# Kernel tuning notes

Hardware: AMD Instinct MI355X
Metric: run time of the kernel (lower is better)

Reference implementation:

```python
import jax, jax.numpy as jnp
import numpy as np

B, N = 256, 512          # trees, nodes per tree (topological order, root last)
IN, HID, OUT = 57, 512, 57  # len(ascii_letters + " .,;'") = 57


def setup_inputs() -> dict:
    rng = np.random.default_rng(0)
    # children indices strictly less than node index; -1 means absent child
    u = rng.random((B, N, 2))
    idx = np.arange(N)[None, :, None]
    ch = np.floor(u * (idx + 1)).astype(np.int32) - 1  # in [-1, i-1]
    left_idx = jnp.asarray(ch[..., 0])
    right_idx = jnp.asarray(ch[..., 1])
    values = jnp.asarray(rng.integers(0, IN, (B, N)), dtype=jnp.int32)
    key = jax.random.key(0)
    k1, k2, k3, k4 = jax.random.split(key, 4)
    s1 = 1.0 / np.sqrt(IN + HID)
    s2 = 1.0 / np.sqrt(HID)
    W_ih = jax.random.uniform(k1, (IN + HID, HID), minval=-s1, maxval=s1, dtype=jnp.float32)
    b_ih = jax.random.uniform(k2, (HID,), minval=-s1, maxval=s1, dtype=jnp.float32)
    W_o = jax.random.uniform(k3, (HID, OUT), minval=-s2, maxval=s2, dtype=jnp.float32)
    b_o = jax.random.uniform(k4, (OUT,), minval=-s2, maxval=s2, dtype=jnp.float32)
    return dict(left_idx=left_idx, right_idx=right_idx, values=values,
                W_ih=W_ih, b_ih=b_ih, W_o=W_o, b_o=b_o)


def _encode(left_idx, right_idx, values, W_ih, b_ih):
    # one-hot chars, precompute the input half of the concat+linear for all nodes
    X = jax.nn.one_hot(values, IN, dtype=W_ih.dtype)        # [B,N,IN]
    Wx, Wh = W_ih[:IN], W_ih[IN:]                            # split concat linear
    Xp = jnp.einsum('bni,ih->bnh', X, Wx) + b_ih             # [B,N,HID]
    SENT = N  # sentinel row holding zeros (hidden for None child)
    li = jnp.where(left_idx < 0, SENT, left_idx)             # [B,N]
    ri = jnp.where(right_idx < 0, SENT, right_idx)
    H0 = jnp.zeros((B, N + 1, HID), Xp.dtype)
    brange = jnp.arange(B)

    def step(H, inp):
        i, xp, l, r = inp                                    # xp:[B,HID], l/r:[B]
        hl = H[brange, l]                                    # gather child hiddens
        hr = H[brange, r]
        h = jnp.tanh(xp + (hl + hr) @ Wh)                    # recurrence
        H = H.at[:, i].set(h)
        return H, None

    xs = (jnp.arange(N), jnp.swapaxes(Xp, 0, 1), li.T, ri.T)
    H, _ = jax.lax.scan(step, H0, xs)
    return H[:, N - 1]                                       # root hidden [B,HID]


def reference(left_idx, right_idx, values, W_ih, b_ih, W_o, b_o):
    h_root = _encode(left_idx, right_idx, values, W_ih, b_ih)
    logits = h_root @ W_o + b_o                              # i2o
    return jax.nn.log_softmax(logits, axis=1)                # [B,OUT]
```

## Files before the change

kernel.cpp:

```cpp
#include <hip/hip_runtime.h>
#include <stdint.h>

#define BATCH 256
#define NNODE 512
#define INP   57
#define HIDD  512
#define OUTD  57

typedef int i32x4 __attribute__((ext_vector_type(4)));

__global__ void pack_wq(const float* __restrict__ W_ih, const float* __restrict__ b_ih,
                        signed char* __restrict__ Wq){
  int idx = blockIdx.x * 256 + threadIdx.x;
  int j    =  idx        & 15;
  int lane = (idx >> 4)  & 63;
  int nt   = (idx >> 10) & 31;
  int kt   =  idx >> 15;
  int n    = nt * 16 + (lane & 15);
  int ksub = (lane >> 4) * 16 + j;
  const float scale = 127.0f * sqrtf((float)(INP + HIDD));
  float wv; float sc = scale;
  if (kt < 8)            wv = W_ih[(size_t)(INP + kt * 64 + ksub) * HIDD + n];
  else {
    sc = scale * 0.5f;
    if (ksub < INP)      wv = W_ih[(size_t)ksub * HIDD + n];
    else if (ksub == INP) wv = b_ih[n];
    else                 wv = 0.0f;
  }
  float q = rintf(wv * sc);
  q = fminf(127.0f, fmaxf(-127.0f, q));
  Wq[idx] = (signed char)q;
}

__device__ __forceinline__ unsigned int avg_s8x4(unsigned int a, unsigned int b){
#if __has_builtin(__builtin_amdgcn_lerp)
  return __builtin_amdgcn_lerp(a ^ 0x80808080u, b ^ 0x80808080u, 0x01010101u) ^ 0x80808080u;
#else
  unsigned int au = a ^ 0x80808080u, bu = b ^ 0x80808080u;
  unsigned int o = au | bu, x = au ^ bu;
  return ((o - ((x >> 1) & 0x7F7F7F7Fu)) ^ 0x80808080u);
#endif
}

struct Pref { uint4 l[2]; uint4 r[2]; };

__device__ __forceinline__ Pref load_pref(
    int m0, int Mcur, int w, int m16, int quad,
    const int* ord_s, const int* li_s, const int* ri_s,
    const signed char* Hb)
{
  Pref p;
  const int koff = w * 64 + quad * 16;
  #pragma unroll
  for (int mt = 0; mt < 2; ++mt) {
    const int row  = mt * 16 + m16;
    const int node = (row < Mcur) ? ord_s[m0 + row] : -1;
    const int loff = (node >= 0) ? li_s[node] : NNODE * HIDD;
    p.l[mt] = *(const uint4*)(Hb + (size_t)(loff + koff));
    const int roff = (node >= 0) ? ri_s[node] : NNODE * HIDD;
    p.r[mt] = *(const uint4*)(Hb + (size_t)(roff + koff));
  }
  return p;
}

__device__ __forceinline__ void write_pref(
    const Pref& p, int m0, int Mcur, int w, int lane, int m16, int quad,
    signed char* __restrict__ Ab, const int* ord_s, const int* val_s)
{
  #pragma unroll
  for (int mt = 0; mt < 2; ++mt) {
    uint4 o;
    o.x = avg_s8x4(p.l[mt].x, p.r[mt].x);
    o.y = avg_s8x4(p.l[mt].y, p.r[mt].y);
    o.z = avg_s8x4(p.l[mt].z, p.r[mt].z);
    o.w = avg_s8x4(p.l[mt].w, p.r[mt].w);
    *(uint4*)(Ab + (w * 2 + mt) * 1024 + lane * 16) = o;
  }
  if (w < 2) {
    const int erow  = w * 16 + m16;
    const int enode = (erow < Mcur) ? ord_s[m0 + erow] : -1;
    const int v     = (enode >= 0) ? val_s[enode] : -1;
    signed char bytes[16];
    #pragma unroll
    for (int j = 0; j < 16; ++j) {
      const int ks = quad * 16 + j;
      bytes[j] = (enode >= 0 && (ks == v || ks == INP)) ? (signed char)127 : (signed char)0;
    }
    *(i32x4*)(Ab + (16 + w) * 1024 + lane * 16) = *(const i32x4*)bytes;
  }
}

template<int NMT>
__device__ __forceinline__ void compute_chunk(
    int m0, int Mcur, int w, int lane, int m16, int quad,
    const signed char* __restrict__ Ab,
    const int* ordoff_s, const i32x4 (&Bv)[9][4], signed char* Hb)
{
  i32x4 acc[NMT][4];
  #pragma unroll
  for (int mt = 0; mt < NMT; ++mt)
    #pragma unroll
    for (int nt = 0; nt < 4; ++nt)
      acc[mt][nt] = (i32x4){0, 0, 0, 0};

  #pragma unroll
  for (int kt = 0; kt < 8; ++kt) {
    #pragma unroll
    for (int mt = 0; mt < NMT; ++mt) {
      i32x4 a = *(const i32x4*)(Ab + (kt * 2 + mt) * 1024 + lane * 16);
      #pragma unroll
      for (int nt = 0; nt < 4; ++nt)
        acc[mt][nt] = __builtin_amdgcn_mfma_i32_16x16x64_i8(a, Bv[kt][nt], acc[mt][nt], 0, 0, 0);
    }
  }
  #pragma unroll
  for (int mt = 0; mt < NMT; ++mt) {
    i32x4 ax = *(const i32x4*)(Ab + (16 + mt) * 1024 + lane * 16);
    #pragma unroll
    for (int nt = 0; nt < 4; ++nt)
      acc[mt][nt] = __builtin_amdgcn_mfma_i32_16x16x64_i8(ax, Bv[8][nt], acc[mt][nt], 0, 0, 0);
  }

  const float SCLE = 5.7707801635558536f / (16129.0f * sqrtf((float)(INP + HIDD)));
  #pragma unroll
  for (int mt = 0; mt < NMT; ++mt) {
    #pragma unroll
    for (int rg = 0; rg < 4; ++rg) {
      const int rowc = mt * 16 + quad * 4 + rg;
      if (rowc < Mcur) {
        signed char* hp = Hb + (size_t)ordoff_s[m0 + rowc] + (w * 64 + m16);
        #pragma unroll
        for (int nt = 0; nt < 4; ++nt) {
          const float x  = (float)acc[mt][nt][rg] * SCLE;
          const float e  = __builtin_amdgcn_exp2f(x);
          const float r  = __builtin_amdgcn_rcpf(e + 1.0f);
          const float tq = fmaf(-254.0f, r, 127.0f);
          hp[nt * 16] = (signed char)__float2int_rn(tq);
        }
      }
    }
  }
}

__global__ __launch_bounds__(512, 2) void tree_rnn(
    const int* __restrict__ left, const int* __restrict__ right,
    const int* __restrict__ values,
    const float* __restrict__ W_ih, const float* __restrict__ b_ih,
    const float* __restrict__ W_o,  const float* __restrict__ b_o,
    const signed char* __restrict__ Wq,
    signed char* __restrict__ Hbuf, float* __restrict__ out)
{
  __shared__ __align__(16) signed char Abuf[2][18 * 1024];
  __shared__ int li_s[NNODE], ri_s[NNODE], val_s[NNODE];
  __shared__ int lvl_s[NNODE], ord_s[NNODE], ordoff_s[NNODE];
  __shared__ int cnt_s[NNODE], cnt2_s[NNODE];
  __shared__ int offs_s[NNODE + 1];
  __shared__ int chg_s, lmax_s;
  __shared__ float hroot_s[HIDD];
  __shared__ float red_s[OUTD][8];
  __shared__ float logit_s[64];

  const int b    = blockIdx.x;
  const int tid  = threadIdx.x;
  const int lane = tid & 63;
  const int w    = tid >> 6;
  signed char* Hb = Hbuf + (size_t)b * (NNODE + 1) * HIDD;

  li_s[tid]  = left  [b * NNODE + tid];
  ri_s[tid]  = right [b * NNODE + tid];
  val_s[tid] = values[b * NNODE + tid];
  lvl_s[tid] = 0; cnt_s[tid] = 0; cnt2_s[tid] = 0;
  if (tid < 128) ((unsigned int*)(Hb + (size_t)NNODE * HIDD))[tid] = 0;
  if (tid == 0) lmax_s = 0;
  __syncthreads();

  for (;;) {
    if (tid == 0) chg_s = 0;
    __syncthreads();
    {
      int l = li_s[tid], r = ri_s[tid];
      int dl = (l >= 0) ? lvl_s[l] : -1;
      int dr = (r >= 0) ? lvl_s[r] : -1;
      int nl = 1 + (dl > dr ? dl : dr);
      if (nl > lvl_s[tid]) { lvl_s[tid] = nl; chg_s = 1; }
    }
    __syncthreads();
    if (!chg_s) break;
  }

  const int myl = lvl_s[tid];
  {
    int ml = myl;
    #pragma unroll
    for (int m = 1; m < 64; m <<= 1) ml = max(ml, __shfl_xor(ml, m, 64));
    if (lane == 0) atomicMax(&lmax_s, ml);
    atomicAdd(&cnt_s[myl], 1);
  }
  __syncthreads();
  const int Lmax = lmax_s;
  if (tid == 0) {
    int acc = 0;
    for (int L = 0; L <= Lmax; ++L) { offs_s[L] = acc; acc += cnt_s[L]; }
    offs_s[Lmax + 1] = acc;
  }
  __syncthreads();
  {
    int pos = offs_s[myl] + atomicAdd(&cnt2_s[myl], 1);
    ord_s[pos] = tid;
    ordoff_s[pos] = tid * HIDD;
  }
  __syncthreads();
  {
    int l = li_s[tid], r = ri_s[tid];
    li_s[tid] = (l < 0 ? NNODE : l) * HIDD;
    ri_s[tid] = (r < 0 ? NNODE : r) * HIDD;
  }

  const int m16  = lane & 15;
  const int quad = lane >> 4;

  i32x4 Bv[9][4];
  #pragma unroll
  for (int kt = 0; kt < 9; ++kt)
    #pragma unroll
    for (int nt = 0; nt < 4; ++nt)
      Bv[kt][nt] = *(const i32x4*)(Wq + ((size_t)(kt * 32 + 4 * w + nt) * 64 + lane) * 16);

  for (int L = 0; L <= Lmax; ++L) {
    const int start = offs_s[L], end = offs_s[L + 1];
    const int nch = (end - start + 31) >> 5;
    __syncthreads();
    {
      Pref p0 = load_pref(start, min(32, end - start), w, m16, quad,
                          ord_s, li_s, ri_s, Hb);
      write_pref(p0, start, min(32, end - start), w, lane, m16, quad,
                 Abuf[0], ord_s, val_s);
    }
    for (int c = 0; c < nch; ++c) {
      __syncthreads();
      const int m0 = start + c * 32;
      const int Mc = min(32, end - m0);
      Pref p;
      const bool more = (c + 1 < nch);
      if (more)
        p = load_pref(m0 + 32, min(32, end - m0 - 32), w, m16, quad,
                      ord_s, li_s, ri_s, Hb);
      const signed char* Ab = Abuf[c & 1];
      if (Mc > 16)
        compute_chunk<2>(m0, Mc, w, lane, m16, quad, Ab, ordoff_s, Bv, Hb);
      else
        compute_chunk<1>(m0, Mc, w, lane, m16, quad, Ab, ordoff_s, Bv, Hb);
      if (more)
        write_pref(p, m0 + 32, min(32, end - m0 - 32), w, lane, m16, quad,
                   Abuf[(c + 1) & 1], ord_s, val_s);
    }
  }
  __syncthreads();

  hroot_s[tid] = (float)Hb[(size_t)(NNODE - 1) * HIDD + tid] * (1.0f / 127.0f);
  __syncthreads();
  {
    const int j = tid >> 3, part = tid & 7;
    if (j < OUTD) {
      float p = 0.f;
      const int k0 = part * 64;
      for (int k = k0; k < k0 + 64; ++k)
        p += hroot_s[k] * W_o[(size_t)k * OUTD + j];
      red_s[j][part] = p;
    }
  }
  __syncthreads();
  if (tid < OUTD) {
    float s = b_o[tid];
    #pragma unroll
    for (int p = 0; p < 8; ++p) s += red_s[tid][p];
    logit_s[tid] = s;
  }
  __syncthreads();
  if (w == 0) {
    float x = (lane < OUTD) ? logit_s[lane] : -1e30f;
    float mx = x;
    #pragma unroll
    for (int m = 1; m < 64; m <<= 1) mx = fmaxf(mx, __shfl_xor(mx, m, 64));
    float ex = (lane < OUTD) ? __expf(x - mx) : 0.f;
    float sm = ex;
    #pragma unroll
    for (int m = 1; m < 64; m <<= 1) sm += __shfl_xor(sm, m, 64);
    float ls = logf(sm);
    if (lane < OUTD) out[b * OUTD + lane] = x - mx - ls;
  }
}

extern "C" void kernel_launch(void* const* d_in, const int* in_sizes, int n_in,
                              void* d_out, int out_size, void* d_ws, size_t ws_size,
                              hipStream_t stream) {
  const int*   left   = (const int*)  d_in[0];
  const int*   right  = (const int*)  d_in[1];
  const int*   values = (const int*)  d_in[2];
  const float* W_ih   = (const float*)d_in[3];
  const float* b_ih   = (const float*)d_in[4];
  const float* W_o    = (const float*)d_in[5];
  const float* b_o    = (const float*)d_in[6];
  float* out = (float*)d_out;

  signed char* Wq   = (signed char*)d_ws;
  signed char* Hbuf = (signed char*)((char*)d_ws + 512 * 1024);

  pack_wq<<<1152, 256, 0, stream>>>(W_ih, b_ih, Wq);
  tree_rnn<<<BATCH, 512, 0, stream>>>(left, right, values, W_ih, b_ih, W_o, b_o,
                                      Wq, Hbuf, out);
}
```

Measured before the change: 212.5 us.

## Prefetch next level's first chunk across level boundaries, patching only dependent child rows

Flattens the per-level chunk loop into one global list of chunk descriptors, so gathering the children of the next chunk can overlap the current chunk's MFMA compute even when the next chunk starts a new level. Children computed in the immediately preceding level are marked "hot" and reloaded after the barrier, while all other children are prefetched early. This hides the gather latency at level starts. The cost is extra shared-memory tables, an extra serial descriptor build on one thread, and extra barriers on first chunks. It also drops the lerp builtin path in favour of the bit-trick average.

```diff
diff --git a/kernel.cpp b/kernel.cpp
--- a/kernel.cpp
+++ b/kernel.cpp
@@ -6,6 +6,7 @@
 #define INP   57
 #define HIDD  512
 #define OUTD  57
+#define SENTOFF (NNODE * HIDD)
 
 typedef int i32x4 __attribute__((ext_vector_type(4)));
 
@@ -33,34 +34,31 @@
 }
 
 __device__ __forceinline__ unsigned int avg_s8x4(unsigned int a, unsigned int b){
-#if __has_builtin(__builtin_amdgcn_lerp)
-  return __builtin_amdgcn_lerp(a ^ 0x80808080u, b ^ 0x80808080u, 0x01010101u) ^ 0x80808080u;
-#else
   unsigned int au = a ^ 0x80808080u, bu = b ^ 0x80808080u;
   unsigned int o = au | bu, x = au ^ bu;
   return ((o - ((x >> 1) & 0x7F7F7F7Fu)) ^ 0x80808080u);
-#endif
 }
 
 struct Pref { uint4 l[2]; uint4 r[2]; };
 
-__device__ __forceinline__ Pref load_pref(
-    int m0, int Mcur, int w, int m16, int quad,
-    const int* ord_s, const int* li_s, const int* ri_s,
+__device__ __forceinline__ void load_pref_safe(
+    Pref& p, int m0, int Mcur, int w, int m16, int quad,
+    const int* ord_s, const int* li_s, const int* ri_s, const int* hot_s,
     const signed char* Hb)
 {
-  Pref p;
   const int koff = w * 64 + quad * 16;
   #pragma unroll
   for (int mt = 0; mt < 2; ++mt) {
     const int row  = mt * 16 + m16;
-    const int node = (row < Mcur) ? ord_s[m0 + row] : -1;
-    const int loff = (node >= 0) ? li_s[node] : NNODE * HIDD;
-    p.l[mt] = *(const uint4*)(Hb + (size_t)(loff + koff));
-    const int roff = (node >= 0) ? ri_s[node] : NNODE * HIDD;
-    p.r[mt] = *(const uint4*)(Hb + (size_t)(roff + koff));
-  }
-  return p;
+    const bool live = row < Mcur;
+    const int pos  = m0 + row;
+    const int node = live ? ord_s[pos] : -1;
+    const int hb   = live ? hot_s[pos] : 0;
+    const int loff = (node >= 0) ? li_s[node] : SENTOFF;
+    const int roff = (node >= 0) ? ri_s[node] : SENTOFF;
+    if (!(hb & 1)) p.l[mt] = *(const uint4*)(Hb + (size_t)(loff + koff));
+    if (!(hb & 2)) p.r[mt] = *(const uint4*)(Hb + (size_t)(roff + koff));
+  }
 }
 
 __device__ __forceinline__ void write_pref(
@@ -90,6 +88,37 @@
   }
 }
 
+__device__ __forceinline__ void patch_and_write(
+    Pref& p, int m0, int Mcur, int w, int lane, int m16, int quad,
+    signed char* __restrict__ Ab,
+    const int* ord_s, const int* li_s, const int* ri_s, const int* val_s,
+    const int* hot_s, const signed char* Hb)
+{
+  const int koff = w * 64 + quad * 16;
+  #pragma unroll
+  for (int mt = 0; mt < 2; ++mt) {
+    const int row  = mt * 16 + m16;
+    const bool live = row < Mcur;
+    const int pos  = m0 + row;
+    const int hb   = live ? hot_s[pos] : 0;
+    if (hb) {
+      const int node = ord_s[pos];
+      if (hb & 1) p.l[mt] = *(const uint4*)(Hb + (size_t)(li_s[node] + koff));
+      if (hb & 2) p.r[mt] = *(const uint4*)(Hb + (size_t)(ri_s[node] + koff));
+    }
+  }
+  write_pref(p, m0, Mcur, w, lane, m16, quad, Ab, ord_s, val_s);
+}
+
+#define SCLE_VAL (5.7707801635558536f / (16129.0f * 23.853720883753127f))
+
+__device__ __forceinline__ void epi_store(int accv, signed char* hp){
+  const float x  = (float)accv * SCLE_VAL;
+  const float e  = __builtin_amdgcn_exp2f(x);
+  const float r  = __builtin_amdgcn_rcpf(e + 1.0f);
+  *hp = (signed char)__float2int_rn(fmaf(-254.0f, r, 127.0f));
+}
+
 template<int NMT>
 __device__ __forceinline__ void compute_chunk(
     int m0, int Mcur, int w, int lane, int m16, int quad,
@@ -121,7 +150,6 @@
       acc[mt][nt] = __builtin_amdgcn_mfma_i32_16x16x64_i8(ax, Bv[8][nt], acc[mt][nt], 0, 0, 0);
   }
 
-  const float SCLE = 5.7707801635558536f / (16129.0f * sqrtf((float)(INP + HIDD)));
   #pragma unroll
   for (int mt = 0; mt < NMT; ++mt) {
     #pragma unroll
@@ -130,13 +158,8 @@
       if (rowc < Mcur) {
         signed char* hp = Hb + (size_t)ordoff_s[m0 + rowc] + (w * 64 + m16);
         #pragma unroll
-        for (int nt = 0; nt < 4; ++nt) {
-          const float x  = (float)acc[mt][nt][rg] * SCLE;
-          const float e  = __builtin_amdgcn_exp2f(x);
-          const float r  = __builtin_amdgcn_rcpf(e + 1.0f);
-          const float tq = fmaf(-254.0f, r, 127.0f);
-          hp[nt * 16] = (signed char)__float2int_rn(tq);
-        }
+        for (int nt = 0; nt < 4; ++nt)
+          epi_store(acc[mt][nt][rg], hp + nt * 16);
       }
     }
   }
@@ -152,10 +175,11 @@
 {
   __shared__ __align__(16) signed char Abuf[2][18 * 1024];
   __shared__ int li_s[NNODE], ri_s[NNODE], val_s[NNODE];
-  __shared__ int lvl_s[NNODE], ord_s[NNODE], ordoff_s[NNODE];
+  __shared__ int lvl_s[NNODE], ord_s[NNODE], ordoff_s[NNODE], hot_s[NNODE];
   __shared__ int cnt_s[NNODE], cnt2_s[NNODE];
   __shared__ int offs_s[NNODE + 1];
-  __shared__ int chg_s, lmax_s;
+  __shared__ int cdesc_s[NNODE];
+  __shared__ int chg_s, lmax_s, nc_s;
   __shared__ float hroot_s[HIDD];
   __shared__ float red_s[OUTD][8];
   __shared__ float logit_s[64];
@@ -202,6 +226,13 @@
     int acc = 0;
     for (int L = 0; L <= Lmax; ++L) { offs_s[L] = acc; acc += cnt_s[L]; }
     offs_s[Lmax + 1] = acc;
+    int nc = 0;
+    for (int L = 0; L <= Lmax; ++L)
+      for (int m0 = offs_s[L]; m0 < offs_s[L + 1]; m0 += 32) {
+        int sz = min(32, offs_s[L + 1] - m0);
+        cdesc_s[nc++] = m0 | (sz << 16) | ((m0 == offs_s[L]) ? (1 << 30) : 0);
+      }
+    nc_s = nc;
   }
   __syncthreads();
   {
@@ -211,10 +242,22 @@
   }
   __syncthreads();
   {
+    const int node = ord_s[tid];
+    const int L = lvl_s[node];
+    const int l = li_s[node], r = ri_s[node];
+    const bool first = (tid - offs_s[L]) < 32;
+    int h = 0;
+    if (first && l >= 0 && lvl_s[l] == L - 1) h |= 1;
+    if (first && r >= 0 && lvl_s[r] == L - 1) h |= 2;
+    hot_s[tid] = h;
+  }
+  __syncthreads();
+  {
     int l = li_s[tid], r = ri_s[tid];
     li_s[tid] = (l < 0 ? NNODE : l) * HIDD;
     ri_s[tid] = (r < 0 ? NNODE : r) * HIDD;
   }
+  __syncthreads();
 
   const int m16  = lane & 15;
   const int quad = lane >> 4;
@@ -226,34 +269,38 @@
     for (int nt = 0; nt < 4; ++nt)
       Bv[kt][nt] = *(const i32x4*)(Wq + ((size_t)(kt * 32 + 4 * w + nt) * 64 + lane) * 16);
 
-  for (int L = 0; L <= Lmax; ++L) {
-    const int start = offs_s[L], end = offs_s[L + 1];
-    const int nch = (end - start + 31) >> 5;
+  const int NC = nc_s;
+  Pref p;
+  {
+    const int d = cdesc_s[0];
+    load_pref_safe(p, d & 0xFFFF, (d >> 16) & 0x3FFF, w, m16, quad,
+                   ord_s, li_s, ri_s, hot_s, Hb);
+  }
+  for (int gc = 0; gc < NC; ++gc) {
+    const int d  = cdesc_s[gc];
+    const int m0 = d & 0xFFFF, Mc = (d >> 16) & 0x3FFF;
+    const bool first = (d >> 30) & 1;
     __syncthreads();
-    {
-      Pref p0 = load_pref(start, min(32, end - start), w, m16, quad,
-                          ord_s, li_s, ri_s, Hb);
-      write_pref(p0, start, min(32, end - start), w, lane, m16, quad,
-                 Abuf[0], ord_s, val_s);
-    }
-    for (int c = 0; c < nch; ++c) {
+    if (first) {
+      patch_and_write(p, m0, Mc, w, lane, m16, quad, Abuf[gc & 1],
+                      ord_s, li_s, ri_s, val_s, hot_s, Hb);
       __syncthreads();
-      const int m0 = start + c * 32;
-      const int Mc = min(32, end - m0);
-      Pref p;
-      const bool more = (c + 1 < nch);
-      if (more)
-        p = load_pref(m0 + 32, min(32, end - m0 - 32), w, m16, quad,
-                      ord_s, li_s, ri_s, Hb);
-      const signed char* Ab = Abuf[c & 1];
-      if (Mc > 16)
-        compute_chunk<2>(m0, Mc, w, lane, m16, quad, Ab, ordoff_s, Bv, Hb);
-      else
-        compute_chunk<1>(m0, Mc, w, lane, m16, quad, Ab, ordoff_s, Bv, Hb);
-      if (more)
-        write_pref(p, m0 + 32, min(32, end - m0 - 32), w, lane, m16, quad,
-                   Abuf[(c + 1) & 1], ord_s, val_s);
-    }
+    }
+    const bool more = gc + 1 < NC;
+    Pref pn; int m01 = 0, Mc1 = 0; bool f1 = false;
+    if (more) {
+      const int d1 = cdesc_s[gc + 1];
+      m01 = d1 & 0xFFFF; Mc1 = (d1 >> 16) & 0x3FFF; f1 = (d1 >> 30) & 1;
+      load_pref_safe(pn, m01, Mc1, w, m16, quad, ord_s, li_s, ri_s, hot_s, Hb);
+    }
+    const signed char* Ab = Abuf[gc & 1];
+    if (Mc > 16)
+      compute_chunk<2>(m0, Mc, w, lane, m16, quad, Ab, ordoff_s, Bv, Hb);
+    else
+      compute_chunk<1>(m0, Mc, w, lane, m16, quad, Ab, ordoff_s, Bv, Hb);
+    if (more && !f1)
+      write_pref(pn, m01, Mc1, w, lane, m16, quad, Abuf[(gc + 1) & 1], ord_s, val_s);
+    p = pn;
   }
   __syncthreads();
 
@@ -262,18 +309,18 @@
   {
     const int j = tid >> 3, part = tid & 7;
     if (j < OUTD) {
-      float p = 0.f;
+      float p2 = 0.f;
       const int k0 = part * 64;
       for (int k = k0; k < k0 + 64; ++k)
-        p += hroot_s[k] * W_o[(size_t)k * OUTD + j];
-      red_s[j][part] = p;
+        p2 += hroot_s[k] * W_o[(size_t)k * OUTD + j];
+      red_s[j][part] = p2;
     }
   }
   __syncthreads();
   if (tid < OUTD) {
     float s = b_o[tid];
     #pragma unroll
-    for (int p = 0; p < 8; ++p) s += red_s[tid][p];
+    for (int pp = 0; pp < 8; ++pp) s += red_s[tid][pp];
     logit_s[tid] = s;
   }
   __syncthreads();
```

Result: faster. 205.3 us (-3.4%).
